# Optimization experiments

Measured on AMD Instinct MI355X. Metric: run time of the kernel, lower is better.

Reference implementation:

```python
import jax, jax.numpy as jnp
import numpy as np

D_TENSOR = 64
SCALE = float(np.sqrt(D_TENSOR))


def setup_inputs() -> dict:
    key = jax.random.key(0)
    kq, kk, kv = jax.random.split(key, 3)
    shape = (1, 16, 4096, 64)  # [B, H, S, D]
    return {
        "q": jax.random.normal(kq, shape, dtype=jnp.float32),
        "k": jax.random.normal(kk, shape, dtype=jnp.float32),
        "v": jax.random.normal(kv, shape, dtype=jnp.float32),
    }


def reference(q, k, v):
    # attn = softmax(q @ k^T / sqrt(d)); output = attn @ v  (no mask, dropout=0/eval)
    scores = jnp.einsum("bhqd,bhkd->bhqk", q, k) / SCALE  # [B,H,S,S]
    attn = jax.nn.softmax(scores, axis=-1)
    output = jnp.einsum("bhqk,bhkd->bhqd", attn, v)       # [B,H,S,D]
    return (output, attn)
```

## Files before the change

### kernel.cpp

```cpp
#include <hip/hip_runtime.h>
#include <hip/hip_bf16.h>


#define NH  16
#define SEQ 4096
#define DH  64
#define BM  128
#define BN  64
#define NKT (SEQ / BN)
#define NRB (SEQ / BM)
#define NT  512

typedef __attribute__((ext_vector_type(8))) short bf16x8;
typedef __attribute__((ext_vector_type(4))) float f32x4;

static __device__ __forceinline__ unsigned short f2bf(float f) {
  unsigned x = __float_as_uint(f);
  return (unsigned short)((x + 0x7fffu + ((x >> 16) & 1u)) >> 16);
}

static __device__ __forceinline__ void bar_lgkm() {
  asm volatile("s_waitcnt lgkmcnt(0)" ::: "memory");
  __builtin_amdgcn_s_barrier();
  asm volatile("" ::: "memory");
}

static __device__ __forceinline__ int swz(int row, int col) {
  return row * 64 + (col ^ ((row & 7) << 3));
}


__global__ __launch_bounds__(NT, 4)
void attn_fused(const float* __restrict__ q, const float* __restrict__ kg,
                const float* __restrict__ vg, float* __restrict__ out,
                float* __restrict__ attn)
{
  __shared__ __align__(16) unsigned short Ks[2][64 * 64];
  __shared__ __align__(16) unsigned short Vt[2][64 * 64];
  __shared__ __align__(16) unsigned short Pb[8][16 * 64];

  const int nwg = NH * NRB;
  int bid = blockIdx.x;
  int wg = (bid & 7) * (nwg >> 3) + (bid >> 3);
  const int h    = wg >> 5;
  const int row0 = (wg & (NRB - 1)) * BM;

  const int t    = threadIdx.x;
  const int lane = t & 63;
  const int wid  = t >> 6;
  const int r16  = lane & 15;
  const int g4   = lane >> 4;

  const float* qh = q  + (size_t)h * SEQ * DH;
  const float* kh = kg + (size_t)h * SEQ * DH;
  const float* vh = vg + (size_t)h * SEQ * DH;

  const int kKey = t >> 4;
  const int kD   = (t & 15) * 4;
  const int vKey = t & 31;
  const int vD   = (t >> 5) * 4;

  const float QS = 0.125f * 1.44269504088896340736f;
  bf16x8 qa[2];
  #pragma unroll
  for (int kf = 0; kf < 2; ++kf) {
    const float* qp = qh + (size_t)(row0 + wid * 16 + r16) * DH + kf * 32 + g4 * 8;
    float4 x0 = *(const float4*)qp;
    float4 x1 = *(const float4*)(qp + 4);
    bf16x8 a;
    a[0] = (short)f2bf(x0.x * QS); a[1] = (short)f2bf(x0.y * QS);
    a[2] = (short)f2bf(x0.z * QS); a[3] = (short)f2bf(x0.w * QS);
    a[4] = (short)f2bf(x1.x * QS); a[5] = (short)f2bf(x1.y * QS);
    a[6] = (short)f2bf(x1.z * QS); a[7] = (short)f2bf(x1.w * QS);
    qa[kf] = a;
  }

  float rsum = 0.f;
  float4 kr[2];
  #pragma unroll
  for (int i = 0; i < 2; ++i)
    kr[i] = *(const float4*)(kh + (size_t)(kKey + 32 * i) * DH + kD);

  #pragma unroll 1
  for (int kt = 0; kt < NKT; ++kt) {
    const int b = kt & 1;
    #pragma unroll
    for (int i = 0; i < 2; ++i)
      *(short4*)&Ks[b][swz(kKey + 32 * i, kD)] =
          make_short4((short)f2bf(kr[i].x), (short)f2bf(kr[i].y),
                      (short)f2bf(kr[i].z), (short)f2bf(kr[i].w));
    if (kt + 1 < NKT) {
      #pragma unroll
      for (int i = 0; i < 2; ++i)
        kr[i] = *(const float4*)(kh + (size_t)((kt + 1) * BN + kKey + 32 * i) * DH + kD);
    }
    bar_lgkm();
    #pragma unroll
    for (int n = 0; n < 4; ++n) {
      bf16x8 a0 = *(const bf16x8*)&Ks[b][swz(n * 16 + r16, g4 * 8)];
      bf16x8 a1 = *(const bf16x8*)&Ks[b][swz(n * 16 + r16, 32 + g4 * 8)];
      f32x4 c = {0.f, 0.f, 0.f, 0.f};
      c = __builtin_amdgcn_mfma_f32_16x16x32_bf16(a0, qa[0], c, 0, 0, 0);
      c = __builtin_amdgcn_mfma_f32_16x16x32_bf16(a1, qa[1], c, 0, 0, 0);
      #pragma unroll
      for (int r = 0; r < 4; ++r) rsum += __builtin_amdgcn_exp2f(c[r]);
    }
  }

  rsum += __shfl_xor(rsum, 16);
  rsum += __shfl_xor(rsum, 32);
  const float inv = 1.0f / rsum;

  f32x4 accO[4];
  #pragma unroll
  for (int n = 0; n < 4; ++n) accO[n] = (f32x4){0.f, 0.f, 0.f, 0.f};

  float4 kr2[2], vr[2];
  #pragma unroll
  for (int i = 0; i < 2; ++i) {
    kr2[i] = *(const float4*)(kh + (size_t)(kKey + 32 * i) * DH + kD);
    vr[i]  = *(const float4*)(vh + (size_t)(vKey + 32 * i) * DH + vD);
  }
  __syncthreads();

  float* aprow = attn + (size_t)(h * SEQ + row0 + wid * 16 + r16) * SEQ;

  #pragma unroll 1
  for (int kt = 0; kt < NKT; ++kt) {
    const int b = kt & 1;
    #pragma unroll
    for (int i = 0; i < 2; ++i) {
      *(short4*)&Ks[b][swz(kKey + 32 * i, kD)] =
          make_short4((short)f2bf(kr2[i].x), (short)f2bf(kr2[i].y),
                      (short)f2bf(kr2[i].z), (short)f2bf(kr2[i].w));
      Vt[b][swz(vD + 0, vKey + 32 * i)] = f2bf(vr[i].x);
      Vt[b][swz(vD + 1, vKey + 32 * i)] = f2bf(vr[i].y);
      Vt[b][swz(vD + 2, vKey + 32 * i)] = f2bf(vr[i].z);
      Vt[b][swz(vD + 3, vKey + 32 * i)] = f2bf(vr[i].w);
    }
    if (kt + 1 < NKT) {
      #pragma unroll
      for (int i = 0; i < 2; ++i) {
        kr2[i] = *(const float4*)(kh + (size_t)((kt + 1) * BN + kKey + 32 * i) * DH + kD);
        vr[i]  = *(const float4*)(vh + (size_t)((kt + 1) * BN + vKey + 32 * i) * DH + vD);
      }
    }
    bar_lgkm();

    #pragma unroll
    for (int n = 0; n < 4; ++n) {
      bf16x8 a0 = *(const bf16x8*)&Ks[b][swz(n * 16 + r16, g4 * 8)];
      bf16x8 a1 = *(const bf16x8*)&Ks[b][swz(n * 16 + r16, 32 + g4 * 8)];
      f32x4 c = {0.f, 0.f, 0.f, 0.f};
      c = __builtin_amdgcn_mfma_f32_16x16x32_bf16(a0, qa[0], c, 0, 0, 0);
      c = __builtin_amdgcn_mfma_f32_16x16x32_bf16(a1, qa[1], c, 0, 0, 0);
      f32x4 p;
      p[0] = __builtin_amdgcn_exp2f(c[0]) * inv;
      p[1] = __builtin_amdgcn_exp2f(c[1]) * inv;
      p[2] = __builtin_amdgcn_exp2f(c[2]) * inv;
      p[3] = __builtin_amdgcn_exp2f(c[3]) * inv;
      __builtin_nontemporal_store(p, (f32x4*)(aprow + (size_t)kt * BN + n * 16 + g4 * 4));
      *(short4*)&Pb[wid][swz(r16, n * 16 + g4 * 4)] =
          make_short4((short)f2bf(p[0]), (short)f2bf(p[1]),
                      (short)f2bf(p[2]), (short)f2bf(p[3]));
    }
    bf16x8 pa0 = *(const bf16x8*)&Pb[wid][swz(r16, g4 * 8)];
    bf16x8 pa1 = *(const bf16x8*)&Pb[wid][swz(r16, 32 + g4 * 8)];
    #pragma unroll
    for (int n = 0; n < 4; ++n) {
      bf16x8 v0 = *(const bf16x8*)&Vt[b][swz(n * 16 + r16, g4 * 8)];
      bf16x8 v1 = *(const bf16x8*)&Vt[b][swz(n * 16 + r16, 32 + g4 * 8)];
      accO[n] = __builtin_amdgcn_mfma_f32_16x16x32_bf16(pa0, v0, accO[n], 0, 0, 0);
      accO[n] = __builtin_amdgcn_mfma_f32_16x16x32_bf16(pa1, v1, accO[n], 0, 0, 0);
    }
  }

  #pragma unroll
  for (int n = 0; n < 4; ++n) {
    #pragma unroll
    for (int r = 0; r < 4; ++r) {
      __builtin_nontemporal_store(accO[n][r],
          out + (size_t)(h * SEQ + row0 + wid * 16 + g4 * 4 + r) * DH + n * 16 + r16);
    }
  }
}

extern "C" void kernel_launch(void* const* d_in, const int* in_sizes, int n_in,
                              void* d_out, int out_size, void* d_ws, size_t ws_size,
                              hipStream_t stream) {
  const float* q = (const float*)d_in[0];
  const float* k = (const float*)d_in[1];
  const float* v = (const float*)d_in[2];
  float* out  = (float*)d_out;
  float* attn = out + (size_t)NH * SEQ * DH;
  hipLaunchKernelGGL(attn_fused, dim3(NH * NRB), dim3(NT), 0, stream,
                     q, k, v, out, attn);
}
```

Baseline: 364.3 us.

## Specialize warps into K/V producers and 32-row compute consumers

Splits the 8 waves into 4 producer waves that load and convert K/V tiles into shared memory one tile ahead, and 4 consumer waves that each handle 32 query rows with two MFMA row fragments. This separates global-load latency from the MFMA/exp/attn-store work and reuses each K/V fragment read across two query fragments. The cost is that only half the waves do compute and write the large attn matrix, and consumers now carry twice the register state, so occupancy or store throughput may suffer.

```diff
diff --git a/kernel.cpp b/kernel.cpp
--- a/kernel.cpp
+++ b/kernel.cpp
@@ -37,7 +37,7 @@
 {
   __shared__ __align__(16) unsigned short Ks[2][64 * 64];
   __shared__ __align__(16) unsigned short Vt[2][64 * 64];
-  __shared__ __align__(16) unsigned short Pb[8][16 * 64];
+  __shared__ __align__(16) unsigned short Pb[4][32 * 64];
 
   const int nwg = NH * NRB;
   int bid = blockIdx.x;
@@ -50,137 +50,214 @@
   const int wid  = t >> 6;
   const int r16  = lane & 15;
   const int g4   = lane >> 4;
+  const bool producer = (wid >= 4);
 
   const float* qh = q  + (size_t)h * SEQ * DH;
   const float* kh = kg + (size_t)h * SEQ * DH;
   const float* vh = vg + (size_t)h * SEQ * DH;
 
-  const int kKey = t >> 4;
-  const int kD   = (t & 15) * 4;
-  const int vKey = t & 31;
-  const int vD   = (t >> 5) * 4;
-
-  const float QS = 0.125f * 1.44269504088896340736f;
-  bf16x8 qa[2];
-  #pragma unroll
-  for (int kf = 0; kf < 2; ++kf) {
-    const float* qp = qh + (size_t)(row0 + wid * 16 + r16) * DH + kf * 32 + g4 * 8;
-    float4 x0 = *(const float4*)qp;
-    float4 x1 = *(const float4*)(qp + 4);
-    bf16x8 a;
-    a[0] = (short)f2bf(x0.x * QS); a[1] = (short)f2bf(x0.y * QS);
-    a[2] = (short)f2bf(x0.z * QS); a[3] = (short)f2bf(x0.w * QS);
-    a[4] = (short)f2bf(x1.x * QS); a[5] = (short)f2bf(x1.y * QS);
-    a[6] = (short)f2bf(x1.z * QS); a[7] = (short)f2bf(x1.w * QS);
-    qa[kf] = a;
-  }
-
-  float rsum = 0.f;
-  float4 kr[2];
-  #pragma unroll
-  for (int i = 0; i < 2; ++i)
-    kr[i] = *(const float4*)(kh + (size_t)(kKey + 32 * i) * DH + kD);
+  const int pt = t - 256;
+  const int pk = (pt & 255) >> 4;
+  const int pd = (t & 15) * 4;
+
+  bf16x8 qa[2][2];
+  if (!producer) {
+    const float QS = 0.125f * 1.44269504088896340736f;
+    #pragma unroll
+    for (int qf = 0; qf < 2; ++qf) {
+      #pragma unroll
+      for (int kf = 0; kf < 2; ++kf) {
+        const float* qp = qh + (size_t)(row0 + wid * 32 + qf * 16 + r16) * DH + kf * 32 + g4 * 8;
+        float4 x0 = *(const float4*)qp;
+        float4 x1 = *(const float4*)(qp + 4);
+        bf16x8 a;
+        a[0] = (short)f2bf(x0.x * QS); a[1] = (short)f2bf(x0.y * QS);
+        a[2] = (short)f2bf(x0.z * QS); a[3] = (short)f2bf(x0.w * QS);
+        a[4] = (short)f2bf(x1.x * QS); a[5] = (short)f2bf(x1.y * QS);
+        a[6] = (short)f2bf(x1.z * QS); a[7] = (short)f2bf(x1.w * QS);
+        qa[qf][kf] = a;
+      }
+    }
+  }
+
+  float4 kr[4], vr[4];
+
+  float rsum0 = 0.f, rsum1 = 0.f;
+
+  if (producer) {
+    #pragma unroll
+    for (int i = 0; i < 4; ++i)
+      kr[i] = *(const float4*)(kh + (size_t)(i * 16 + pk) * DH + pd);
+    #pragma unroll
+    for (int i = 0; i < 4; ++i)
+      *(short4*)&Ks[0][swz(i * 16 + pk, pd)] =
+          make_short4((short)f2bf(kr[i].x), (short)f2bf(kr[i].y),
+                      (short)f2bf(kr[i].z), (short)f2bf(kr[i].w));
+    #pragma unroll
+    for (int i = 0; i < 4; ++i)
+      kr[i] = *(const float4*)(kh + (size_t)(BN + i * 16 + pk) * DH + pd);
+  }
+  bar_lgkm();
 
   #pragma unroll 1
   for (int kt = 0; kt < NKT; ++kt) {
-    const int b = kt & 1;
-    #pragma unroll
-    for (int i = 0; i < 2; ++i)
-      *(short4*)&Ks[b][swz(kKey + 32 * i, kD)] =
+    if (producer) {
+      if (kt < NKT - 1) {
+        #pragma unroll
+        for (int i = 0; i < 4; ++i)
+          *(short4*)&Ks[(kt + 1) & 1][swz(i * 16 + pk, pd)] =
+              make_short4((short)f2bf(kr[i].x), (short)f2bf(kr[i].y),
+                          (short)f2bf(kr[i].z), (short)f2bf(kr[i].w));
+        if (kt < NKT - 2) {
+          #pragma unroll
+          for (int i = 0; i < 4; ++i)
+            kr[i] = *(const float4*)(kh + (size_t)((kt + 2) * BN + i * 16 + pk) * DH + pd);
+        }
+      }
+    } else {
+      const int b = kt & 1;
+      #pragma unroll
+      for (int n = 0; n < 4; ++n) {
+        bf16x8 a0 = *(const bf16x8*)&Ks[b][swz(n * 16 + r16, g4 * 8)];
+        bf16x8 a1 = *(const bf16x8*)&Ks[b][swz(n * 16 + r16, 32 + g4 * 8)];
+        f32x4 c0 = {0.f, 0.f, 0.f, 0.f};
+        f32x4 c1 = {0.f, 0.f, 0.f, 0.f};
+        c0 = __builtin_amdgcn_mfma_f32_16x16x32_bf16(a0, qa[0][0], c0, 0, 0, 0);
+        c0 = __builtin_amdgcn_mfma_f32_16x16x32_bf16(a1, qa[0][1], c0, 0, 0, 0);
+        c1 = __builtin_amdgcn_mfma_f32_16x16x32_bf16(a0, qa[1][0], c1, 0, 0, 0);
+        c1 = __builtin_amdgcn_mfma_f32_16x16x32_bf16(a1, qa[1][1], c1, 0, 0, 0);
+        #pragma unroll
+        for (int r = 0; r < 4; ++r) {
+          rsum0 += __builtin_amdgcn_exp2f(c0[r]);
+          rsum1 += __builtin_amdgcn_exp2f(c1[r]);
+        }
+      }
+    }
+    bar_lgkm();
+  }
+
+  float inv0 = 0.f, inv1 = 0.f;
+  if (!producer) {
+    rsum0 += __shfl_xor(rsum0, 16); rsum0 += __shfl_xor(rsum0, 32);
+    rsum1 += __shfl_xor(rsum1, 16); rsum1 += __shfl_xor(rsum1, 32);
+    inv0 = 1.0f / rsum0;
+    inv1 = 1.0f / rsum1;
+  }
+
+  f32x4 accO[2][4];
+  #pragma unroll
+  for (int qf = 0; qf < 2; ++qf)
+    #pragma unroll
+    for (int n = 0; n < 4; ++n) accO[qf][n] = (f32x4){0.f, 0.f, 0.f, 0.f};
+
+  if (producer) {
+    #pragma unroll
+    for (int i = 0; i < 4; ++i) {
+      kr[i] = *(const float4*)(kh + (size_t)(i * 16 + pk) * DH + pd);
+      vr[i] = *(const float4*)(vh + (size_t)(i * 16 + pk) * DH + pd);
+    }
+    #pragma unroll
+    for (int i = 0; i < 4; ++i) {
+      *(short4*)&Ks[0][swz(i * 16 + pk, pd)] =
           make_short4((short)f2bf(kr[i].x), (short)f2bf(kr[i].y),
                       (short)f2bf(kr[i].z), (short)f2bf(kr[i].w));
-    if (kt + 1 < NKT) {
-      #pragma unroll
-      for (int i = 0; i < 2; ++i)
-        kr[i] = *(const float4*)(kh + (size_t)((kt + 1) * BN + kKey + 32 * i) * DH + kD);
-    }
-    bar_lgkm();
-    #pragma unroll
-    for (int n = 0; n < 4; ++n) {
-      bf16x8 a0 = *(const bf16x8*)&Ks[b][swz(n * 16 + r16, g4 * 8)];
-      bf16x8 a1 = *(const bf16x8*)&Ks[b][swz(n * 16 + r16, 32 + g4 * 8)];
-      f32x4 c = {0.f, 0.f, 0.f, 0.f};
-      c = __builtin_amdgcn_mfma_f32_16x16x32_bf16(a0, qa[0], c, 0, 0, 0);
-      c = __builtin_amdgcn_mfma_f32_16x16x32_bf16(a1, qa[1], c, 0, 0, 0);
-      #pragma unroll
-      for (int r = 0; r < 4; ++r) rsum += __builtin_amdgcn_exp2f(c[r]);
-    }
-  }
-
-  rsum += __shfl_xor(rsum, 16);
-  rsum += __shfl_xor(rsum, 32);
-  const float inv = 1.0f / rsum;
-
-  f32x4 accO[4];
-  #pragma unroll
-  for (int n = 0; n < 4; ++n) accO[n] = (f32x4){0.f, 0.f, 0.f, 0.f};
-
-  float4 kr2[2], vr[2];
-  #pragma unroll
-  for (int i = 0; i < 2; ++i) {
-    kr2[i] = *(const float4*)(kh + (size_t)(kKey + 32 * i) * DH + kD);
-    vr[i]  = *(const float4*)(vh + (size_t)(vKey + 32 * i) * DH + vD);
-  }
-  __syncthreads();
-
-  float* aprow = attn + (size_t)(h * SEQ + row0 + wid * 16 + r16) * SEQ;
+      Vt[0][swz(pd + 0, i * 16 + pk)] = f2bf(vr[i].x);
+      Vt[0][swz(pd + 1, i * 16 + pk)] = f2bf(vr[i].y);
+      Vt[0][swz(pd + 2, i * 16 + pk)] = f2bf(vr[i].z);
+      Vt[0][swz(pd + 3, i * 16 + pk)] = f2bf(vr[i].w);
+    }
+    #pragma unroll
+    for (int i = 0; i < 4; ++i) {
+      kr[i] = *(const float4*)(kh + (size_t)(BN + i * 16 + pk) * DH + pd);
+      vr[i] = *(const float4*)(vh + (size_t)(BN + i * 16 + pk) * DH + pd);
+    }
+  }
+  bar_lgkm();
+
+  float* ap0 = attn + (size_t)(h * SEQ + row0 + wid * 32 + r16) * SEQ;
+  float* ap1 = ap0 + (size_t)16 * SEQ;
 
   #pragma unroll 1
   for (int kt = 0; kt < NKT; ++kt) {
-    const int b = kt & 1;
-    #pragma unroll
-    for (int i = 0; i < 2; ++i) {
-      *(short4*)&Ks[b][swz(kKey + 32 * i, kD)] =
-          make_short4((short)f2bf(kr2[i].x), (short)f2bf(kr2[i].y),
-                      (short)f2bf(kr2[i].z), (short)f2bf(kr2[i].w));
-      Vt[b][swz(vD + 0, vKey + 32 * i)] = f2bf(vr[i].x);
-      Vt[b][swz(vD + 1, vKey + 32 * i)] = f2bf(vr[i].y);
-      Vt[b][swz(vD + 2, vKey + 32 * i)] = f2bf(vr[i].z);
-      Vt[b][swz(vD + 3, vKey + 32 * i)] = f2bf(vr[i].w);
-    }
-    if (kt + 1 < NKT) {
-      #pragma unroll
-      for (int i = 0; i < 2; ++i) {
-        kr2[i] = *(const float4*)(kh + (size_t)((kt + 1) * BN + kKey + 32 * i) * DH + kD);
-        vr[i]  = *(const float4*)(vh + (size_t)((kt + 1) * BN + vKey + 32 * i) * DH + vD);
+    if (producer) {
+      if (kt < NKT - 1) {
+        const int b1 = (kt + 1) & 1;
+        #pragma unroll
+        for (int i = 0; i < 4; ++i) {
+          *(short4*)&Ks[b1][swz(i * 16 + pk, pd)] =
+              make_short4((short)f2bf(kr[i].x), (short)f2bf(kr[i].y),
+                          (short)f2bf(kr[i].z), (short)f2bf(kr[i].w));
+          Vt[b1][swz(pd + 0, i * 16 + pk)] = f2bf(vr[i].x);
+          Vt[b1][swz(pd + 1, i * 16 + pk)] = f2bf(vr[i].y);
+          Vt[b1][swz(pd + 2, i * 16 + pk)] = f2bf(vr[i].z);
+          Vt[b1][swz(pd + 3, i * 16 + pk)] = f2bf(vr[i].w);
+        }
+        if (kt < NKT - 2) {
+          #pragma unroll
+          for (int i = 0; i < 4; ++i) {
+            kr[i] = *(const float4*)(kh + (size_t)((kt + 2) * BN + i * 16 + pk) * DH + pd);
+            vr[i] = *(const float4*)(vh + (size_t)((kt + 2) * BN + i * 16 + pk) * DH + pd);
+          }
+        }
+      }
+    } else {
+      const int b = kt & 1;
+      #pragma unroll
+      for (int n = 0; n < 4; ++n) {
+        bf16x8 a0 = *(const bf16x8*)&Ks[b][swz(n * 16 + r16, g4 * 8)];
+        bf16x8 a1 = *(const bf16x8*)&Ks[b][swz(n * 16 + r16, 32 + g4 * 8)];
+        f32x4 c0 = {0.f, 0.f, 0.f, 0.f};
+        f32x4 c1 = {0.f, 0.f, 0.f, 0.f};
+        c0 = __builtin_amdgcn_mfma_f32_16x16x32_bf16(a0, qa[0][0], c0, 0, 0, 0);
+        c0 = __builtin_amdgcn_mfma_f32_16x16x32_bf16(a1, qa[0][1], c0, 0, 0, 0);
+        c1 = __builtin_amdgcn_mfma_f32_16x16x32_bf16(a0, qa[1][0], c1, 0, 0, 0);
+        c1 = __builtin_amdgcn_mfma_f32_16x16x32_bf16(a1, qa[1][1], c1, 0, 0, 0);
+        f32x4 p0, p1;
+        p0[0] = __builtin_amdgcn_exp2f(c0[0]) * inv0;
+        p0[1] = __builtin_amdgcn_exp2f(c0[1]) * inv0;
+        p0[2] = __builtin_amdgcn_exp2f(c0[2]) * inv0;
+        p0[3] = __builtin_amdgcn_exp2f(c0[3]) * inv0;
+        p1[0] = __builtin_amdgcn_exp2f(c1[0]) * inv1;
+        p1[1] = __builtin_amdgcn_exp2f(c1[1]) * inv1;
+        p1[2] = __builtin_amdgcn_exp2f(c1[2]) * inv1;
+        p1[3] = __builtin_amdgcn_exp2f(c1[3]) * inv1;
+        __builtin_nontemporal_store(p0, (f32x4*)(ap0 + (size_t)kt * BN + n * 16 + g4 * 4));
+        __builtin_nontemporal_store(p1, (f32x4*)(ap1 + (size_t)kt * BN + n * 16 + g4 * 4));
+        *(short4*)&Pb[wid][swz(r16, n * 16 + g4 * 4)] =
+            make_short4((short)f2bf(p0[0]), (short)f2bf(p0[1]),
+                        (short)f2bf(p0[2]), (short)f2bf(p0[3]));
+        *(short4*)&Pb[wid][swz(16 + r16, n * 16 + g4 * 4)] =
+            make_short4((short)f2bf(p1[0]), (short)f2bf(p1[1]),
+                        (short)f2bf(p1[2]), (short)f2bf(p1[3]));
+      }
+      bf16x8 pa00 = *(const bf16x8*)&Pb[wid][swz(r16, g4 * 8)];
+      bf16x8 pa01 = *(const bf16x8*)&Pb[wid][swz(r16, 32 + g4 * 8)];
+      bf16x8 pa10 = *(const bf16x8*)&Pb[wid][swz(16 + r16, g4 * 8)];
+      bf16x8 pa11 = *(const bf16x8*)&Pb[wid][swz(16 + r16, 32 + g4 * 8)];
+      #pragma unroll
+      for (int n = 0; n < 4; ++n) {
+        bf16x8 v0 = *(const bf16x8*)&Vt[b][swz(n * 16 + r16, g4 * 8)];
+        bf16x8 v1 = *(const bf16x8*)&Vt[b][swz(n * 16 + r16, 32 + g4 * 8)];
+        accO[0][n] = __builtin_amdgcn_mfma_f32_16x16x32_bf16(pa00, v0, accO[0][n], 0, 0, 0);
+        accO[0][n] = __builtin_amdgcn_mfma_f32_16x16x32_bf16(pa01, v1, accO[0][n], 0, 0, 0);
+        accO[1][n] = __builtin_amdgcn_mfma_f32_16x16x32_bf16(pa10, v0, accO[1][n], 0, 0, 0);
+        accO[1][n] = __builtin_amdgcn_mfma_f32_16x16x32_bf16(pa11, v1, accO[1][n], 0, 0, 0);
       }
     }
     bar_lgkm();
-
-    #pragma unroll
-    for (int n = 0; n < 4; ++n) {
-      bf16x8 a0 = *(const bf16x8*)&Ks[b][swz(n * 16 + r16, g4 * 8)];
-      bf16x8 a1 = *(const bf16x8*)&Ks[b][swz(n * 16 + r16, 32 + g4 * 8)];
-      f32x4 c = {0.f, 0.f, 0.f, 0.f};
-      c = __builtin_amdgcn_mfma_f32_16x16x32_bf16(a0, qa[0], c, 0, 0, 0);
-      c = __builtin_amdgcn_mfma_f32_16x16x32_bf16(a1, qa[1], c, 0, 0, 0);
-      f32x4 p;
-      p[0] = __builtin_amdgcn_exp2f(c[0]) * inv;
-      p[1] = __builtin_amdgcn_exp2f(c[1]) * inv;
-      p[2] = __builtin_amdgcn_exp2f(c[2]) * inv;
-      p[3] = __builtin_amdgcn_exp2f(c[3]) * inv;
-      __builtin_nontemporal_store(p, (f32x4*)(aprow + (size_t)kt * BN + n * 16 + g4 * 4));
-      *(short4*)&Pb[wid][swz(r16, n * 16 + g4 * 4)] =
-          make_short4((short)f2bf(p[0]), (short)f2bf(p[1]),
-                      (short)f2bf(p[2]), (short)f2bf(p[3]));
-    }
-    bf16x8 pa0 = *(const bf16x8*)&Pb[wid][swz(r16, g4 * 8)];
-    bf16x8 pa1 = *(const bf16x8*)&Pb[wid][swz(r16, 32 + g4 * 8)];
-    #pragma unroll
-    for (int n = 0; n < 4; ++n) {
-      bf16x8 v0 = *(const bf16x8*)&Vt[b][swz(n * 16 + r16, g4 * 8)];
-      bf16x8 v1 = *(const bf16x8*)&Vt[b][swz(n * 16 + r16, 32 + g4 * 8)];
-      accO[n] = __builtin_amdgcn_mfma_f32_16x16x32_bf16(pa0, v0, accO[n], 0, 0, 0);
-      accO[n] = __builtin_amdgcn_mfma_f32_16x16x32_bf16(pa1, v1, accO[n], 0, 0, 0);
-    }
-  }
-
-  #pragma unroll
-  for (int n = 0; n < 4; ++n) {
-    #pragma unroll
-    for (int r = 0; r < 4; ++r) {
-      __builtin_nontemporal_store(accO[n][r],
-          out + (size_t)(h * SEQ + row0 + wid * 16 + g4 * 4 + r) * DH + n * 16 + r16);
+  }
+
+  if (!producer) {
+    #pragma unroll
+    for (int qf = 0; qf < 2; ++qf) {
+      #pragma unroll
+      for (int n = 0; n < 4; ++n) {
+        #pragma unroll
+        for (int r = 0; r < 4; ++r) {
+          __builtin_nontemporal_store(accO[qf][n][r],
+              out + (size_t)(h * SEQ + row0 + wid * 32 + qf * 16 + g4 * 4 + r) * DH + n * 16 + r16);
+        }
+      }
     }
   }
 }
```

Result: slower. 377.0 us (+3.5%).
